# Kernel tuning notes

Measured on AMD Instinct MI355X. Metric: run time of the kernel, lower is better.

Reference implementation:

```python
import jax, jax.numpy as jnp
import numpy as np

B, N, DEG = 64, 1024, 32          # graphs, nodes/graph, avg degree
IN_CH, HID = 128, 128
E = B * N * DEG                    # 2,097,152 edges
K = N // 2                         # TopKPooling ratio=0.5 -> 512 kept per graph


def setup_inputs() -> dict:
    key = jax.random.key(0)
    ks = jax.random.split(key, 10)
    x = jax.random.normal(ks[0], (B * N, IN_CH), jnp.float32)
    # within-graph random edges, then offset to global node ids
    src = jax.random.randint(ks[1], (B, N * DEG), 0, N)
    dst = jax.random.randint(ks[2], (B, N * DEG), 0, N)
    off = (jnp.arange(B) * N)[:, None]
    edge_index = jnp.stack([(src + off).reshape(-1), (dst + off).reshape(-1)]).astype(jnp.int64)
    batch = jnp.repeat(jnp.arange(B), N).astype(jnp.int64)
    g = lambda k, fi, fo: jax.random.normal(k, (fi, fo), jnp.float32) / np.sqrt(fi)
    return dict(
        x=x, edge_index=edge_index, batch=batch,
        W1=g(ks[3], IN_CH, HID), b1=jnp.zeros(HID, jnp.float32),
        W2=g(ks[4], HID, HID),   b2=jnp.zeros(HID, jnp.float32),
        w_pool=jax.random.normal(ks[5], (IN_CH,), jnp.float32) / np.sqrt(IN_CH),
        W3=g(ks[6], HID, HID),   b3=jnp.zeros(HID, jnp.float32),
        W4=g(ks[7], HID, HID),   b4=jnp.zeros(HID, jnp.float32),
    )


def _gin(h, src, dst, valid, Wa, ba, Wb, bb, n):
    # GINConv (eps=0): nn(x + sum_{j->i} x_j); valid masks filtered edges
    msg = jnp.where(valid[:, None], h[jnp.where(valid, src, 0)], 0.0)
    agg = jax.ops.segment_sum(msg, jnp.where(valid, dst, 0), num_segments=n)
    h = agg + h
    return jax.nn.relu(h @ Wa + ba) @ Wb + bb


def reference(x, edge_index, batch, W1, b1, W2, b2, w_pool, W3, b3, W4, b4):
    src, dst = edge_index[0], edge_index[1]
    n = B * N
    all_valid = jnp.ones((E,), bool)

    # conv1 + relu
    out = jax.nn.relu(_gin(x, src, dst, all_valid, W1, b1, W2, b2, n))

    # TopKPooling: score from attn=x (original features), tanh nonlinearity
    score = jnp.tanh((x @ w_pool) / jnp.linalg.norm(w_pool))          # [B*N]
    topv, topi = jax.lax.top_k(score.reshape(B, N), K)                 # per-graph
    perm = (topi + (jnp.arange(B) * N)[:, None]).reshape(-1)           # [B*K] global ids
    out = out[perm] * topv.reshape(-1)[:, None]                        # gate kept nodes

    # relabel edges; keep only edges with both endpoints retained
    new_idx = jnp.full((n,), -1, jnp.int32).at[perm].set(jnp.arange(B * K, dtype=jnp.int32))
    s2, d2 = new_idx[src], new_idx[dst]
    valid = (s2 >= 0) & (d2 >= 0)

    # conv2 + relu on pooled graph
    out = jax.nn.relu(_gin(out, s2, d2, valid, W3, b3, W4, b4, B * K))

    # global_mean_pool: each graph has exactly K kept nodes (contiguous per graph)
    return out.reshape(B, K, HID).mean(axis=1)
```

## Files before the change

### kernel.cpp

```cpp
#include <hip/hip_runtime.h>
#include <hip/hip_bf16.h>

constexpr int B_    = 64;
constexpr int N_    = 1024;
constexpr int DEG_  = 32;
constexpr int CH_   = 128;
constexpr int E_    = B_ * N_ * DEG_;
constexpr int NB_   = B_ * N_;
constexpr int K_    = N_ / 2;
constexpr int NK_   = B_ * K_;
constexpr int EPG_  = N_ * DEG_;
constexpr int CPB_  = 16;
constexpr int CE_   = EPG_ / CPB_;

typedef __attribute__((ext_vector_type(8))) short bf16x8;
typedef __attribute__((ext_vector_type(4))) float f32x4;

template <int NBLOCKS>
__device__ inline int xcd_work(int bid) {
  return (bid & 7) * (NBLOCKS / 8) + (bid >> 3);
}

__device__ inline void split_bf16(float v, unsigned short& h, unsigned short& l) {
  unsigned u = __float_as_uint(v);
  unsigned hr = (u + 0x7FFFu + ((u >> 16) & 1u)) & 0xFFFF0000u;
  h = (unsigned short)(hr >> 16);
  float d = v - __uint_as_float(hr);
  unsigned ud = __float_as_uint(d);
  l = (unsigned short)((ud + 0x7FFFu + ((ud >> 16) & 1u)) >> 16);
}

__global__ __launch_bounds__(256) void scores_kernel(
    const float* __restrict__ x, const float* __restrict__ w_pool,
    float* __restrict__ scores, int n) {
  int wave = (blockIdx.x * blockDim.x + threadIdx.x) >> 6;
  int lane = threadIdx.x & 63;
  if (wave >= n) return;
  float w0 = w_pool[lane], w1 = w_pool[64 + lane];
  float a0 = x[(size_t)wave * CH_ + lane];
  float a1 = x[(size_t)wave * CH_ + 64 + lane];
  float dot = a0 * w0 + a1 * w1;
  float nrm = w0 * w0 + w1 * w1;
  #pragma unroll
  for (int m = 32; m > 0; m >>= 1) {
    dot += __shfl_xor(dot, m, 64);
    nrm += __shfl_xor(nrm, m, 64);
  }
  if (lane == 0) scores[wave] = tanhf(dot / sqrtf(nrm));
}

__global__ __launch_bounds__(1024) void topk_kernel(
    const float* __restrict__ scores, int* __restrict__ perm,
    float* __restrict__ topv, int* __restrict__ new_idx) {
  __shared__ unsigned long long keys[N_];
  int b = blockIdx.x, t = threadIdx.x;
  float f = scores[b * N_ + t];
  unsigned u = __float_as_uint(f);
  u = (u & 0x80000000u) ? ~u : (u | 0x80000000u);
  unsigned du = ~u;
  keys[t] = ((unsigned long long)du << 32) | (unsigned)t;
  __syncthreads();
  for (int size = 2; size <= N_; size <<= 1) {
    for (int stride = size >> 1; stride > 0; stride >>= 1) {
      int j = t ^ stride;
      if (j > t) {
        unsigned long long a = keys[t], bk = keys[j];
        bool asc = ((t & size) == 0);
        if ((a > bk) == asc) { keys[t] = bk; keys[j] = a; }
      }
      __syncthreads();
    }
  }
  int idx = (int)(keys[t] & 0xFFFFFFFFu);
  int g = b * N_ + idx;
  if (t < K_) {
    int r = b * K_ + t;
    perm[r] = g;
    topv[r] = scores[g];
    new_idx[g] = r;
  } else {
    new_idx[g] = -1;
  }
}

__global__ __launch_bounds__(256) void csr_hist_kernel(
    const int* __restrict__ dst, int* __restrict__ ph) {
  __shared__ int hist[N_];
  int c = blockIdx.x, t = threadIdx.x;
  int b = c >> 4;
  reinterpret_cast<int4*>(hist)[t] = make_int4(0, 0, 0, 0);
  __syncthreads();
  const int ebase = b * EPG_ + (c & 15) * CE_;
  const int4* d4 = reinterpret_cast<const int4*>(dst + ebase);
  #pragma unroll
  for (int i = 0; i < 2; ++i) {
    int4 d = d4[t + i * 256];
    atomicAdd(&hist[d.x - b * N_], 1);
    atomicAdd(&hist[d.y - b * N_], 1);
    atomicAdd(&hist[d.z - b * N_], 1);
    atomicAdd(&hist[d.w - b * N_], 1);
  }
  __syncthreads();
  int4* out4 = reinterpret_cast<int4*>(ph + (size_t)c * N_);
  out4[t] = reinterpret_cast<const int4*>(hist)[t];
}

__global__ __launch_bounds__(1024) void csr_scan_kernel(
    int* __restrict__ ph, int* __restrict__ offsets1) {
  __shared__ int wsum[16];
  int b = blockIdx.x, n = threadIdx.x;
  int c[CPB_], pre[CPB_];
  int tot = 0;
  #pragma unroll
  for (int q = 0; q < CPB_; ++q) {
    c[q] = ph[(size_t)(b * CPB_ + q) * N_ + n];
    pre[q] = tot;
    tot += c[q];
  }
  int lane = n & 63;
  int incl = tot;
  #pragma unroll
  for (int d = 1; d < 64; d <<= 1) {
    int v = __shfl_up(incl, d, 64);
    if (lane >= d) incl += v;
  }
  if (lane == 63) wsum[n >> 6] = incl;
  __syncthreads();
  if (n < 16) {
    int wv = wsum[n];
    int wincl = wv;
    #pragma unroll
    for (int d = 1; d < 16; d <<= 1) {
      int v = __shfl_up(wincl, d, 16);
      if ((n & 15) >= d) wincl += v;
    }
    wsum[n] = wincl - wv;
  }
  __syncthreads();
  int excl = incl - tot + wsum[n >> 6];
  int base = b * EPG_ + excl;
  offsets1[b * N_ + n] = base;
  if (b == 0 && n == 0) offsets1[NB_] = E_;
  #pragma unroll
  for (int q = 0; q < CPB_; ++q)
    ph[(size_t)(b * CPB_ + q) * N_ + n] = base + pre[q];
}

__global__ __launch_bounds__(256) void csr_scatter_kernel(
    const int* __restrict__ src, const int* __restrict__ dst,
    const int* __restrict__ ph, const int* __restrict__ new_idx,
    unsigned* __restrict__ csr) {
  __shared__ int cursor[N_];
  int c = blockIdx.x, t = threadIdx.x;
  int b = c >> 4;
  reinterpret_cast<int4*>(cursor)[t] =
      reinterpret_cast<const int4*>(ph + (size_t)c * N_)[t];
  __syncthreads();
  const int ebase = b * EPG_ + (c & 15) * CE_;
  const int nbase = b * N_, kbase = b * K_;
  const int4* s4 = reinterpret_cast<const int4*>(src + ebase);
  const int4* d4 = reinterpret_cast<const int4*>(dst + ebase);
  #pragma unroll
  for (int i = 0; i < 2; ++i) {
    int4 s = s4[t + i * 256];
    int4 d = d4[t + i * 256];
    int n0 = new_idx[s.x], n1 = new_idx[s.y], n2 = new_idx[s.z], n3 = new_idx[s.w];
    unsigned v0 = ((unsigned)(s.x - nbase) << 16) |
                  ((n0 < 0) ? 0xFFFFu : (unsigned)(n0 - kbase));
    unsigned v1 = ((unsigned)(s.y - nbase) << 16) |
                  ((n1 < 0) ? 0xFFFFu : (unsigned)(n1 - kbase));
    unsigned v2 = ((unsigned)(s.z - nbase) << 16) |
                  ((n2 < 0) ? 0xFFFFu : (unsigned)(n2 - kbase));
    unsigned v3 = ((unsigned)(s.w - nbase) << 16) |
                  ((n3 < 0) ? 0xFFFFu : (unsigned)(n3 - kbase));
    int p0 = atomicAdd(&cursor[d.x - nbase], 1); csr[p0] = v0;
    int p1 = atomicAdd(&cursor[d.y - nbase], 1); csr[p1] = v1;
    int p2 = atomicAdd(&cursor[d.z - nbase], 1); csr[p2] = v2;
    int p3 = atomicAdd(&cursor[d.w - nbase], 1); csr[p3] = v3;
  }
}

__global__ __launch_bounds__(256) void wfrag_kernel(
    const float* __restrict__ W1, const float* __restrict__ W2,
    const float* __restrict__ W3, const float* __restrict__ W4,
    unsigned short* __restrict__ whi, unsigned short* __restrict__ wlo) {
  int wid = (blockIdx.x * 256 + (int)threadIdx.x) >> 6;
  int l = threadIdx.x & 63;
  const float* Ws[4] = {W1, W2, W3, W4};
  int mat = wid >> 5, kb = (wid >> 3) & 3, cg = wid & 7;
  const float* W = Ws[mat];
  int col = cg * 16 + (l & 15);
  int kbase = kb * 32 + (l >> 4) * 8;
  bf16x8 hv, lv;
  #pragma unroll
  for (int j = 0; j < 8; ++j) {
    unsigned short h, lo;
    split_bf16(W[(size_t)(kbase + j) * CH_ + col], h, lo);
    hv[j] = (short)h; lv[j] = (short)lo;
  }
  size_t slot = ((size_t)mat * 32 + (size_t)(kb * 8 + cg)) * 64 + l;
  *reinterpret_cast<bf16x8*>(whi + slot * 8) = hv;
  *reinterpret_cast<bf16x8*>(wlo + slot * 8) = lv;
}

__global__ __launch_bounds__(256) void aggregate_kernel(
    const float* __restrict__ feat, const int* __restrict__ offs,
    const unsigned* __restrict__ srcs, float* __restrict__ out) {
  int work = xcd_work<NB_ / 4>(blockIdx.x);
  int node = work * 4 + ((int)threadIdx.x >> 6);
  int lane = threadIdx.x & 63;
  int h = lane >> 5, li = lane & 31;
  int gbase = (node >> 10) << 10;
  const float4* f4 = reinterpret_cast<const float4*>(feat);
  int s = offs[node], e = offs[node + 1];
  int total = (e - s) + 1;
  float4 acc = make_float4(0.f, 0.f, 0.f, 0.f);
  int i = 0;
  if (total >= 2) {
    int j = h ? (gbase + (int)(srcs[s] >> 16)) : node;
    acc = f4[(size_t)j * 32 + li];
    i = 2;
  }
  for (; i + 4 <= total; i += 4) {
    int ja = gbase + (int)(srcs[s + (h ? i : i - 1)] >> 16);
    int jb = gbase + (int)(srcs[s + (h ? i + 2 : i + 1)] >> 16);
    float4 va = f4[(size_t)ja * 32 + li];
    float4 vb = f4[(size_t)jb * 32 + li];
    acc.x += va.x + vb.x; acc.y += va.y + vb.y;
    acc.z += va.z + vb.z; acc.w += va.w + vb.w;
  }
  for (; i + 2 <= total; i += 2) {
    int j = gbase + (int)(srcs[s + (h ? i : i - 1)] >> 16);
    float4 v = f4[(size_t)j * 32 + li];
    acc.x += v.x; acc.y += v.y; acc.z += v.z; acc.w += v.w;
  }
  if (i < total) {
    if (h == 0) {
      int j = (i == 0) ? node : (gbase + (int)(srcs[s + i - 1] >> 16));
      float4 v = f4[(size_t)j * 32 + li];
      acc.x += v.x; acc.y += v.y; acc.z += v.z; acc.w += v.w;
    }
  }
  acc.x += __shfl_xor(acc.x, 32, 64);
  acc.y += __shfl_xor(acc.y, 32, 64);
  acc.z += __shfl_xor(acc.z, 32, 64);
  acc.w += __shfl_xor(acc.w, 32, 64);
  if (h == 0)
    reinterpret_cast<float4*>(out)[(size_t)node * 32 + li] = acc;
}

__global__ __launch_bounds__(256) void aggregate2_kernel(
    const float* __restrict__ pooled, const int* __restrict__ perm,
    const int* __restrict__ offs1, const unsigned* __restrict__ csr,
    float* __restrict__ out) {
  int work = xcd_work<NK_ / 4>(blockIdx.x);
  int r = work * 4 + ((int)threadIdx.x >> 6);
  int lane = threadIdx.x & 63;
  int kbase = (r >> 9) << 9;
  const float2* f2 = reinterpret_cast<const float2*>(pooled);
  int g = perm[r];
  int s = offs1[g], e = offs1[g + 1];
  float2 acc = f2[(size_t)r * 64 + lane];
  int p = s;
  for (; p + 4 <= e; p += 4) {
    short n0 = (short)(csr[p]     & 0xFFFFu);
    short n1 = (short)(csr[p + 1] & 0xFFFFu);
    short n2 = (short)(csr[p + 2] & 0xFFFFu);
    short n3 = (short)(csr[p + 3] & 0xFFFFu);
    if (n0 >= 0) { float2 v = f2[(size_t)(kbase + n0) * 64 + lane]; acc.x += v.x; acc.y += v.y; }
    if (n1 >= 0) { float2 v = f2[(size_t)(kbase + n1) * 64 + lane]; acc.x += v.x; acc.y += v.y; }
    if (n2 >= 0) { float2 v = f2[(size_t)(kbase + n2) * 64 + lane]; acc.x += v.x; acc.y += v.y; }
    if (n3 >= 0) { float2 v = f2[(size_t)(kbase + n3) * 64 + lane]; acc.x += v.x; acc.y += v.y; }
  }
  for (; p < e; ++p) {
    short n0 = (short)(csr[p] & 0xFFFFu);
    if (n0 >= 0) { float2 v = f2[(size_t)(kbase + n0) * 64 + lane]; acc.x += v.x; acc.y += v.y; }
  }
  reinterpret_cast<float2*>(out)[(size_t)r * 64 + lane] = acc;
}

template <bool FINAL>
__global__ __launch_bounds__(256) void gemm_pair_mfma_kernel(
    const float* __restrict__ in,
    const unsigned short* __restrict__ wahi, const unsigned short* __restrict__ walo,
    const float* __restrict__ ba,
    const unsigned short* __restrict__ wbhi, const unsigned short* __restrict__ wblo,
    const float* __restrict__ bb,
    float* __restrict__ out) {
  __shared__ unsigned short Ahi[64 * CH_];
  __shared__ unsigned short Alo[64 * CH_];
  int tid = threadIdx.x;
  int w = tid >> 6, l = tid & 63;
  int block_row = blockIdx.x * 64;

  const float4* in4 = reinterpret_cast<const float4*>(in) + (size_t)block_row * 32;
  #pragma unroll
  for (int i = 0; i < 8; ++i) {
    int idx = tid + i * 256;
    float4 v = in4[idx];
    int row = idx >> 5;
    int byte = row * 256 + (idx & 31) * 8;
    byte ^= (row & 7) << 4;
    unsigned short h0, l0, h1, l1, h2, l2, h3, l3;
    split_bf16(v.x, h0, l0); split_bf16(v.y, h1, l1);
    split_bf16(v.z, h2, l2); split_bf16(v.w, h3, l3);
    uint2 hp, lp;
    hp.x = (unsigned)h0 | ((unsigned)h1 << 16);
    hp.y = (unsigned)h2 | ((unsigned)h3 << 16);
    lp.x = (unsigned)l0 | ((unsigned)l1 << 16);
    lp.y = (unsigned)l2 | ((unsigned)l3 << 16);
    *reinterpret_cast<uint2*>(reinterpret_cast<char*>(Ahi) + byte) = hp;
    *reinterpret_cast<uint2*>(reinterpret_cast<char*>(Alo) + byte) = lp;
  }
  __syncthreads();

  int arow = 16 * w + (l & 15);
  int kb_off = (l >> 4) * 16;
  bf16x8 a1h[4], a1l[4];
  #pragma unroll
  for (int kb = 0; kb < 4; ++kb) {
    int byte = arow * 256 + kb * 64 + kb_off;
    byte ^= (arow & 7) << 4;
    a1h[kb] = *reinterpret_cast<const bf16x8*>(reinterpret_cast<const char*>(Ahi) + byte);
    a1l[kb] = *reinterpret_cast<const bf16x8*>(reinterpret_cast<const char*>(Alo) + byte);
  }
  __syncthreads();

  int colbase = l & 15;
  int rowoff = (l >> 4) * 4;

  #pragma unroll 2
  for (int cg = 0; cg < 8; ++cg) {
    f32x4 acc1 = {0.f, 0.f, 0.f, 0.f};
    f32x4 acc2 = {0.f, 0.f, 0.f, 0.f};
    #pragma unroll
    for (int kb = 0; kb < 4; ++kb) {
      size_t slot = (size_t)(kb * 8 + cg) * 64 + l;
      bf16x8 bh = *reinterpret_cast<const bf16x8*>(wahi + slot * 8);
      bf16x8 bl = *reinterpret_cast<const bf16x8*>(walo + slot * 8);
      acc1 = __builtin_amdgcn_mfma_f32_16x16x32_bf16(a1h[kb], bh, acc1, 0, 0, 0);
      acc1 = __builtin_amdgcn_mfma_f32_16x16x32_bf16(a1h[kb], bl, acc1, 0, 0, 0);
      acc2 = __builtin_amdgcn_mfma_f32_16x16x32_bf16(a1l[kb], bh, acc2, 0, 0, 0);
    }
    int col = cg * 16 + colbase;
    float bv = ba[col];
    #pragma unroll
    for (int r = 0; r < 4; ++r) {
      float t = fmaxf(acc1[r] + acc2[r] + bv, 0.f);
      int trow = 16 * w + rowoff + r;
      int byte = (trow * 256 + col * 2) ^ ((trow & 7) << 4);
      unsigned short th, tl;
      split_bf16(t, th, tl);
      *reinterpret_cast<unsigned short*>(reinterpret_cast<char*>(Ahi) + byte) = th;
      *reinterpret_cast<unsigned short*>(reinterpret_cast<char*>(Alo) + byte) = tl;
    }
  }
  __syncthreads();

  bf16x8 a2h[4], a2l[4];
  #pragma unroll
  for (int kb = 0; kb < 4; ++kb) {
    int byte = arow * 256 + kb * 64 + kb_off;
    byte ^= (arow & 7) << 4;
    a2h[kb] = *reinterpret_cast<const bf16x8*>(reinterpret_cast<const char*>(Ahi) + byte);
    a2l[kb] = *reinterpret_cast<const bf16x8*>(reinterpret_cast<const char*>(Alo) + byte);
  }
  if (FINAL) __syncthreads();

  float* redf = reinterpret_cast<float*>(Ahi);

  #pragma unroll 2
  for (int cg = 0; cg < 8; ++cg) {
    f32x4 acc1 = {0.f, 0.f, 0.f, 0.f};
    f32x4 acc2 = {0.f, 0.f, 0.f, 0.f};
    #pragma unroll
    for (int kb = 0; kb < 4; ++kb) {
      size_t slot = (size_t)(kb * 8 + cg) * 64 + l;
      bf16x8 bh = *reinterpret_cast<const bf16x8*>(wbhi + slot * 8);
      bf16x8 bl = *reinterpret_cast<const bf16x8*>(wblo + slot * 8);
      acc1 = __builtin_amdgcn_mfma_f32_16x16x32_bf16(a2h[kb], bh, acc1, 0, 0, 0);
      acc1 = __builtin_amdgcn_mfma_f32_16x16x32_bf16(a2h[kb], bl, acc1, 0, 0, 0);
      acc2 = __builtin_amdgcn_mfma_f32_16x16x32_bf16(a2l[kb], bh, acc2, 0, 0, 0);
    }
    int col = cg * 16 + colbase;
    float bv = bb[col];
    if (!FINAL) {
      #pragma unroll
      for (int r = 0; r < 4; ++r) {
        float v = fmaxf(acc1[r] + acc2[r] + bv, 0.f);
        out[(size_t)(block_row + 16 * w + rowoff + r) * CH_ + col] = v;
      }
    } else {
      float part = 0.f;
      #pragma unroll
      for (int r = 0; r < 4; ++r)
        part += fmaxf(acc1[r] + acc2[r] + bv, 0.f);
      redf[(w * 4 + (l >> 4)) * CH_ + col] = part;
    }
  }

  if (FINAL) {
    __syncthreads();
    if (tid < CH_) {
      float tot = 0.f;
      #pragma unroll
      for (int s = 0; s < 16; ++s) tot += redf[s * CH_ + tid];
      int b = block_row / K_;
      atomicAdd(&out[b * CH_ + tid], tot * (1.0f / (float)K_));
    }
  }
}

__global__ __launch_bounds__(256) void pool_gather_kernel(
    const float* __restrict__ out1, const int* __restrict__ perm,
    const float* __restrict__ topv, float* __restrict__ pooled) {
  int work = xcd_work<NK_ / 4>(blockIdx.x);
  int r = work * 4 + ((int)threadIdx.x >> 6);
  int lane = threadIdx.x & 63;
  int g = perm[r];
  float v = topv[r];
  float2 t = reinterpret_cast<const float2*>(out1)[(size_t)g * 64 + lane];
  t.x *= v; t.y *= v;
  reinterpret_cast<float2*>(pooled)[(size_t)r * 64 + lane] = t;
}

extern "C" void kernel_launch(void* const* d_in, const int* in_sizes, int n_in,
                              void* d_out, int out_size, void* d_ws, size_t ws_size,
                              hipStream_t stream) {
  const float* x      = (const float*)d_in[0];
  const int*   eidx   = (const int*)d_in[1];
  const int*   src    = eidx;
  const int*   dst    = eidx + E_;
  const float* W1 = (const float*)d_in[3];
  const float* b1 = (const float*)d_in[4];
  const float* W2 = (const float*)d_in[5];
  const float* b2 = (const float*)d_in[6];
  const float* w_pool = (const float*)d_in[7];
  const float* W3 = (const float*)d_in[8];
  const float* b3 = (const float*)d_in[9];
  const float* W4 = (const float*)d_in[10];
  const float* b4 = (const float*)d_in[11];
  float* dout = (float*)d_out;

  char* w = (char*)d_ws;
  auto carve = [&](size_t bytes) {
    char* p = w;
    w += (bytes + 255) & ~(size_t)255;
    return p;
  };
  float*          bufA     = (float*)carve((size_t)NB_ * CH_ * 4);
  float*          bufB     = (float*)carve((size_t)NB_ * CH_ * 4);
  unsigned*       csr      = (unsigned*)carve((size_t)E_ * 4);
  int*            ph       = (int*)  carve((size_t)B_ * CPB_ * N_ * 4);
  int*            offsets1 = (int*)  carve((size_t)(NB_ + 4) * 4);
  float*          scores   = (float*)carve((size_t)NB_ * 4);
  int*            perm     = (int*)  carve((size_t)NK_ * 4);
  float*          topv     = (float*)carve((size_t)NK_ * 4);
  int*            new_idx  = (int*)  carve((size_t)NB_ * 4);
  unsigned short* whiB     = (unsigned short*)carve((size_t)4 * 16384 * 2);
  unsigned short* wloB     = (unsigned short*)carve((size_t)4 * 16384 * 2);
  auto whi = [&](int m) { return whiB + (size_t)m * 16384; };
  auto wlo = [&](int m) { return wloB + (size_t)m * 16384; };

  hipMemsetAsync(dout, 0, (size_t)B_ * CH_ * 4, stream);

  wfrag_kernel<<<32, 256, 0, stream>>>(W1, W2, W3, W4, whiB, wloB);

  scores_kernel<<<NB_ / 4, 256, 0, stream>>>(x, w_pool, scores, NB_);
  topk_kernel<<<B_, 1024, 0, stream>>>(scores, perm, topv, new_idx);

  csr_hist_kernel<<<B_ * CPB_, 256, 0, stream>>>(dst, ph);
  csr_scan_kernel<<<B_, 1024, 0, stream>>>(ph, offsets1);
  csr_scatter_kernel<<<B_ * CPB_, 256, 0, stream>>>(src, dst, ph, new_idx, csr);

  aggregate_kernel<<<NB_ / 4, 256, 0, stream>>>(x, offsets1, csr, bufA);
  gemm_pair_mfma_kernel<false><<<NB_ / 64, 256, 0, stream>>>(
      bufA, whi(0), wlo(0), b1, whi(1), wlo(1), b2, bufB);

  pool_gather_kernel<<<NK_ / 4, 256, 0, stream>>>(bufB, perm, topv, bufA);

  aggregate2_kernel<<<NK_ / 4, 256, 0, stream>>>(bufA, perm, offsets1, csr, bufB);

  gemm_pair_mfma_kernel<true><<<NK_ / 64, 256, 0, stream>>>(
      bufB, whi(2), wlo(2), b3, whi(3), wlo(3), b4, dout);
}
```

Measured before the change: 292.3 us.

## Compact valid neighbors via ballot and use half-wave float4 gathers in pooled aggregation

```diff
diff --git a/kernel.cpp b/kernel.cpp
--- a/kernel.cpp
+++ b/kernel.cpp
@@ -12,6 +12,7 @@
 constexpr int EPG_  = N_ * DEG_;
 constexpr int CPB_  = 16;
 constexpr int CE_   = EPG_ / CPB_;
+constexpr int MAXD_ = 112;
 
 typedef __attribute__((ext_vector_type(8))) short bf16x8;
 typedef __attribute__((ext_vector_type(4))) float f32x4;
@@ -221,6 +222,20 @@
     acc = f4[(size_t)j * 32 + li];
     i = 2;
   }
+  for (; i + 8 <= total; i += 8) {
+    int j0 = gbase + (int)(srcs[s + (h ? i     : i - 1)] >> 16);
+    int j1 = gbase + (int)(srcs[s + (h ? i + 2 : i + 1)] >> 16);
+    int j2 = gbase + (int)(srcs[s + (h ? i + 4 : i + 3)] >> 16);
+    int j3 = gbase + (int)(srcs[s + (h ? i + 6 : i + 5)] >> 16);
+    float4 v0 = f4[(size_t)j0 * 32 + li];
+    float4 v1 = f4[(size_t)j1 * 32 + li];
+    float4 v2 = f4[(size_t)j2 * 32 + li];
+    float4 v3 = f4[(size_t)j3 * 32 + li];
+    acc.x += (v0.x + v1.x) + (v2.x + v3.x);
+    acc.y += (v0.y + v1.y) + (v2.y + v3.y);
+    acc.z += (v0.z + v1.z) + (v2.z + v3.z);
+    acc.w += (v0.w + v1.w) + (v2.w + v3.w);
+  }
   for (; i + 4 <= total; i += 4) {
     int ja = gbase + (int)(srcs[s + (h ? i : i - 1)] >> 16);
     int jb = gbase + (int)(srcs[s + (h ? i + 2 : i + 1)] >> 16);
@@ -253,30 +268,67 @@
     const float* __restrict__ pooled, const int* __restrict__ perm,
     const int* __restrict__ offs1, const unsigned* __restrict__ csr,
     float* __restrict__ out) {
+  __shared__ int ids[4][MAXD_];
   int work = xcd_work<NK_ / 4>(blockIdx.x);
-  int r = work * 4 + ((int)threadIdx.x >> 6);
+  int wv = (int)threadIdx.x >> 6;
+  int r = work * 4 + wv;
   int lane = threadIdx.x & 63;
+  int h = lane >> 5, li = lane & 31;
   int kbase = (r >> 9) << 9;
-  const float2* f2 = reinterpret_cast<const float2*>(pooled);
   int g = perm[r];
   int s = offs1[g], e = offs1[g + 1];
-  float2 acc = f2[(size_t)r * 64 + lane];
-  int p = s;
-  for (; p + 4 <= e; p += 4) {
-    short n0 = (short)(csr[p]     & 0xFFFFu);
-    short n1 = (short)(csr[p + 1] & 0xFFFFu);
-    short n2 = (short)(csr[p + 2] & 0xFFFFu);
-    short n3 = (short)(csr[p + 3] & 0xFFFFu);
-    if (n0 >= 0) { float2 v = f2[(size_t)(kbase + n0) * 64 + lane]; acc.x += v.x; acc.y += v.y; }
-    if (n1 >= 0) { float2 v = f2[(size_t)(kbase + n1) * 64 + lane]; acc.x += v.x; acc.y += v.y; }
-    if (n2 >= 0) { float2 v = f2[(size_t)(kbase + n2) * 64 + lane]; acc.x += v.x; acc.y += v.y; }
-    if (n3 >= 0) { float2 v = f2[(size_t)(kbase + n3) * 64 + lane]; acc.x += v.x; acc.y += v.y; }
-  }
-  for (; p < e; ++p) {
-    short n0 = (short)(csr[p] & 0xFFFFu);
-    if (n0 >= 0) { float2 v = f2[(size_t)(kbase + n0) * 64 + lane]; acc.x += v.x; acc.y += v.y; }
-  }
-  reinterpret_cast<float2*>(out)[(size_t)r * 64 + lane] = acc;
+  int deg = e - s;
+  if (lane == 0) ids[wv][0] = r;
+  int m = 1;
+  for (int base = 0; base < deg; base += 64) {
+    int idx = base + lane;
+    bool val = false;
+    int id = 0;
+    if (idx < deg) {
+      short nl = (short)(csr[s + idx] & 0xFFFFu);
+      val = nl >= 0;
+      id = kbase + nl;
+    }
+    unsigned long long mask = __ballot(val);
+    if (val) {
+      int pos = m + __popcll(mask & ((1ull << lane) - 1ull));
+      ids[wv][pos] = id;
+    }
+    m += __popcll(mask);
+  }
+  const float4* f4 = reinterpret_cast<const float4*>(pooled);
+  float4 acc = make_float4(0.f, 0.f, 0.f, 0.f);
+  int i = 0;
+  for (; i + 8 <= m; i += 8) {
+    int j0 = ids[wv][i     + h];
+    int j1 = ids[wv][i + 2 + h];
+    int j2 = ids[wv][i + 4 + h];
+    int j3 = ids[wv][i + 6 + h];
+    float4 v0 = f4[(size_t)j0 * 32 + li];
+    float4 v1 = f4[(size_t)j1 * 32 + li];
+    float4 v2 = f4[(size_t)j2 * 32 + li];
+    float4 v3 = f4[(size_t)j3 * 32 + li];
+    acc.x += (v0.x + v1.x) + (v2.x + v3.x);
+    acc.y += (v0.y + v1.y) + (v2.y + v3.y);
+    acc.z += (v0.z + v1.z) + (v2.z + v3.z);
+    acc.w += (v0.w + v1.w) + (v2.w + v3.w);
+  }
+  for (; i + 2 <= m; i += 2) {
+    int j = ids[wv][i + h];
+    float4 v = f4[(size_t)j * 32 + li];
+    acc.x += v.x; acc.y += v.y; acc.z += v.z; acc.w += v.w;
+  }
+  if (i < m && h == 0) {
+    int j = ids[wv][i];
+    float4 v = f4[(size_t)j * 32 + li];
+    acc.x += v.x; acc.y += v.y; acc.z += v.z; acc.w += v.w;
+  }
+  acc.x += __shfl_xor(acc.x, 32, 64);
+  acc.y += __shfl_xor(acc.y, 32, 64);
+  acc.z += __shfl_xor(acc.z, 32, 64);
+  acc.w += __shfl_xor(acc.w, 32, 64);
+  if (h == 0)
+    reinterpret_cast<float4*>(out)[(size_t)r * 32 + li] = acc;
 }
 
 template <bool FINAL>
```

Result: faster. 266.9 us (-8.7%).
